# Optimization experiments

Hardware: AMD Instinct MI355X
Metric: run time of the kernel (lower is better)

Reference implementation:

```python
import jax, jax.numpy as jnp
import numpy as np

N_INST = 1_000_000
N_BINS_X = 512
N_BINS_Y = 512
STDDEV_X = 0.6
STDDEV_Y = 0.6
STDDEV_TRUNC = 2.5
NUM_CKSR = 48
NUM_CE = 96
SLICE_CAP = 16
SQRT2 = float(np.sqrt(2.0))
# truncated window spans 2*trunc*stddev = 3.0 bin units -> at most 5 bins per axis
K = 5


def setup_inputs() -> dict:
    key = jax.random.key(0)
    k1, k2, k3, k4, k5 = jax.random.split(key, 5)
    scale = jnp.array([N_BINS_X, N_BINS_Y], dtype=jnp.float32)
    inst_pos = jax.random.uniform(k1, (N_INST, 2), dtype=jnp.float32) * scale
    luts = jax.random.randint(k2, (N_INST,), 0, 7, dtype=jnp.int32)
    luts = jnp.where(luts == 1, 0, luts)  # assert: no LUT has type 1
    ffs = jax.random.randint(k3, (N_INST,), 0, 2, dtype=jnp.int32)
    ffs = jnp.where(luts > 0, 0, ffs)  # an instance is either a LUT or a FF
    cksr = jax.random.randint(k4, (N_INST,), 0, NUM_CKSR, dtype=jnp.int32)
    ce = jax.random.randint(k5, (N_INST,), 0, NUM_CE, dtype=jnp.int32)
    ff_ctrlsets = jnp.stack([cksr, ce], axis=1)
    return {"inst_pos": inst_pos, "is_inst_luts": luts, "is_inst_ffs": ffs,
            "ff_ctrlsets": ff_ctrlsets}


def _axis_weights(pos, stddev, num_bins):
    """Truncated-Gaussian bin overlap weights along one axis.
    pos: (N,) centers in bin units. Returns bins (N,K) int32, weights (N,K)."""
    half = STDDEV_TRUNC * stddev
    lo_bin = jnp.floor(pos - half).astype(jnp.int32)            # (N,)
    bins = lo_bin[:, None] + jnp.arange(K, dtype=jnp.int32)     # (N,K)
    e_lo = bins.astype(pos.dtype)
    e_hi = e_lo + 1.0
    w_lo = (pos - half)[:, None]
    w_hi = (pos + half)[:, None]
    lo_c = jnp.clip(e_lo, w_lo, w_hi)
    hi_c = jnp.clip(e_hi, w_lo, w_hi)
    phi = lambda e: 0.5 * (1.0 + jax.lax.erf((e - pos[:, None]) / (stddev * SQRT2)))
    w = phi(hi_c) - phi(lo_c)
    valid = (bins >= 0) & (bins < num_bins)
    w = jnp.where(valid, w, 0.0)
    w = w / (jnp.sum(w, axis=1, keepdims=True) + 1e-12)  # each inst contributes unit demand
    return jnp.clip(bins, 0, num_bins - 1), w


def reference(inst_pos, is_inst_luts, is_inst_ffs, ff_ctrlsets):
    dt = inst_pos.dtype
    bx, wx = _axis_weights(inst_pos[:, 0], STDDEV_X, N_BINS_X)
    by, wy = _axis_weights(inst_pos[:, 1], STDDEV_Y, N_BINS_Y)
    w2 = wx[:, :, None] * wy[:, None, :]                        # (N,K,K)
    idx = bx[:, :, None] * N_BINS_Y + by[:, None, :]            # (N,K,K) flat bin id
    nb = N_BINS_X * N_BINS_Y

    lut_mask = is_inst_luts > 0
    ff_mask = (is_inst_ffs > 0) & (~lut_mask)

    # LUT demand map (Gaussian splat of LUT instances)
    lut_w = jnp.where(lut_mask[:, None, None], w2, 0.0)
    lut_dem = jnp.zeros(nb, dt).at[idx.reshape(-1)].add(lut_w.reshape(-1))

    # FF demand maps keyed by control sets (cksr shared per half-slice, ce per quarter)
    ff_w = jnp.where(ff_mask[:, None, None], w2, 0.0)
    cksr = ff_ctrlsets[:, 0]
    ce = ff_ctrlsets[:, 1]
    idx_ck = (idx * NUM_CKSR + cksr[:, None, None]).reshape(-1)
    idx_ce = (idx * NUM_CE + ce[:, None, None]).reshape(-1)
    ck_dem = jnp.zeros(nb * NUM_CKSR, dt).at[idx_ck].add(ff_w.reshape(-1))
    ck_dem = ck_dem.reshape(nb, NUM_CKSR)
    ce_dem = jnp.zeros(nb * NUM_CE, dt).at[idx_ce].add(ff_w.reshape(-1))
    ce_dem = ce_dem.reshape(nb, NUM_CE)

    # ultrascale packing rule: half-slice shares CK/SR, quarter-slice shares CE
    half_cap = SLICE_CAP / 2.0
    quarter_cap = SLICE_CAP / 4.0
    eff_ck = jnp.sum(jnp.ceil(ck_dem / half_cap), axis=1) * half_cap
    eff_ce = jnp.sum(jnp.ceil(ce_dem / quarter_cap), axis=1) * quarter_cap
    ff_eff = jnp.maximum(eff_ck, eff_ce)        # effective FF capacity consumed per bin
    ff_raw = jnp.sum(ck_dem, axis=1)            # raw FF demand per bin
    ff_scale = jnp.maximum(ff_eff / jnp.maximum(ff_raw, 1e-6), 1.0)
    lut_scale = jnp.maximum(lut_dem / SLICE_CAP, 1.0)

    # gather per-instance inflated resource area with the same Gaussian weights
    lut_area = jnp.sum(w2 * lut_scale[idx], axis=(1, 2))
    ff_area = jnp.sum(w2 * ff_scale[idx], axis=(1, 2))
    zero = jnp.zeros((), dt)
    return jnp.where(lut_mask, lut_area, zero) + jnp.where(ff_mask, ff_area, zero)
```

## Files before the change

kernel.cpp:

```cpp
#include <hip/hip_runtime.h>

#define N_INST   1000000
#define NBX      512
#define NBY      512
#define NB       (NBX * NBY)
#define NUM_CKSR 48
#define NUM_CE   96
#define K        4

#define FTX   16
#define FTY   8
#define TGX   (NBX / FTX)
#define TGY   (NBY / FTY)
#define NFT   (TGX * TGY)
#define NBLK  512
#define NPER  (NFT / NBLK)
#define SUB   8
#define CAPL  96
#define CAPF  48
#define RS    145
#define ACCW  (FTX * FTY * RS)
#define PXW   20
#define PYW   12
#define PW    (PXW * PYW)

#define CSTRIDE 16

#define KHALF  ((float)(2.5 * 0.6))
#define KDENOM ((float)(0.6 * 1.4142135623730951))

__device__ __forceinline__ void axis_weights4(float pos, int nbins, int& lo_out, float w[K]) {
    float wlo = pos - KHALF;
    float whi = pos + KHALF;
    int lo_bin = (int)floorf(wlo);
    lo_out = lo_bin;
    float phi[K + 1];
#pragma unroll
    for (int k = 0; k <= K; ++k) {
        float e = (float)(lo_bin + k);
        float ec = fminf(fmaxf(e, wlo), whi);
        phi[k] = 0.5f * (1.f + erff((ec - pos) / KDENOM));
    }
    float wsum = 0.f;
#pragma unroll
    for (int k = 0; k < K; ++k) {
        int b = lo_bin + k;
        float ww = phi[k + 1] - phi[k];
        if (b < 0 || b >= nbins) ww = 0.f;
        w[k] = ww;
        wsum += ww;
    }
    float d = wsum + 1e-12f;
#pragma unroll
    for (int k = 0; k < K; ++k) w[k] = w[k] / d;
}

__device__ __forceinline__ unsigned q10(float w) {
    return min(1023u, (unsigned)rintf(w * 1024.f));
}

__global__ void __launch_bounds__(256) classify_kernel(
        const float* __restrict__ pos,
        const int* __restrict__ luts,
        const int* __restrict__ ffs,
        const int* __restrict__ ctrl,
        int* __restrict__ lut_cur,
        int* __restrict__ ff_cur,
        uint4* __restrict__ lutb,
        float4* __restrict__ ffwx,
        float4* __restrict__ ffwy,
        unsigned* __restrict__ ffmeta) {
    int i = blockIdx.x * blockDim.x + threadIdx.x;
    if (i >= N_INST) return;
    int sb = blockIdx.x & (SUB - 1);
    bool is_lut = luts[i] > 0;
    bool is_ff  = !is_lut && (ffs[i] > 0);
    if (!is_lut && !is_ff) return;

    float px = pos[2 * i], py = pos[2 * i + 1];
    int lox, loy;
    float wx[K], wy[K];
    axis_weights4(px, NBX, lox, wx);
    axis_weights4(py, NBY, loy, wy);

    if (is_lut) {
        unsigned qx[4] = { q10(wx[0]), q10(wx[1]), q10(wx[2]), q10(wx[3]) };
        unsigned qy[4] = { q10(wy[0]), q10(wy[1]), q10(wy[2]), q10(wy[3]) };
        int tx = ((int)px) >> 4, ty = ((int)py) >> 3;
        unsigned rx = (unsigned)(lox - tx * FTX + 2);
        unsigned ry = (unsigned)(loy - ty * FTY + 2);
        uint4 e;
        e.x = qx[0] | (qx[1] << 10) | (qx[2] << 20);
        e.y = qx[3] | (qy[0] << 10) | (qy[1] << 20);
        e.z = qy[2] | (qy[3] << 10);
        e.w = rx | (ry << 5);
        int sbk = (tx * TGY + ty) * SUB + sb;
        int slot = atomicAdd(&lut_cur[sbk * CSTRIDE], 1);
        if (slot < CAPL) lutb[(size_t)sbk * CAPL + slot] = e;
        return;
    }

    float4 w1 = make_float4(wx[0], wx[1], wx[2], wx[3]);
    float4 w2 = make_float4(wy[0], wy[1], wy[2], wy[3]);
    unsigned ck   = (unsigned)ctrl[2 * i];
    unsigned ce48 = 48u + (unsigned)ctrl[2 * i + 1];
    int tx0 = max(lox, 0) >> 4, tx1 = min(lox + 3, NBX - 1) >> 4;
    int ty0 = max(loy, 0) >> 3, ty1 = min(loy + 3, NBY - 1) >> 3;
    for (int tx = tx0; tx <= tx1; ++tx) {
        for (int ty = ty0; ty <= ty1; ++ty) {
            unsigned cx = (unsigned)(lox - tx * FTX + 4);
            unsigned cy = (unsigned)(loy - ty * FTY + 4);
            int sbk = (tx * TGY + ty) * SUB + sb;
            int slot = atomicAdd(&ff_cur[sbk * CSTRIDE], 1);
            if (slot < CAPF) {
                size_t idx = (size_t)sbk * CAPF + slot;
                ffwx[idx] = w1;
                ffwy[idx] = w2;
                ffmeta[idx] = ck | (ce48 << 6) | (cx << 14) | (cy << 19);
            }
        }
    }
}

__global__ void __launch_bounds__(1024) tile_kernel(
        const uint4* __restrict__ lutb,
        const float4* __restrict__ ffwx,
        const float4* __restrict__ ffwy,
        const unsigned* __restrict__ ffmeta,
        const int* __restrict__ lut_cur,
        const int* __restrict__ ff_cur,
        float* __restrict__ lut_dem,
        float* __restrict__ ff_scale) {
    __shared__ float acc[ACCW];
    __shared__ unsigned patch[PW];
    __shared__ int cnt_s[2 * SUB];
    __shared__ int lpre[SUB + 1], fpre[SUB + 1];
    int tid = threadIdx.x;

    for (int tt = 0; tt < NPER; ++tt) {
        int t = blockIdx.x + tt * NBLK;
        int X0 = (t / TGY) * FTX;
        int Y0 = (t % TGY) * FTY;

        if (tid < SUB)
            cnt_s[tid] = min(lut_cur[(t * SUB + tid) * CSTRIDE], CAPL);
        else if (tid < 2 * SUB)
            cnt_s[tid] = min(ff_cur[(t * SUB + (tid - SUB)) * CSTRIDE], CAPF);

        for (int j = tid; j < ACCW; j += 1024) acc[j] = 0.f;
        if (tid < PW) patch[tid] = 0u;
        __syncthreads();

        if (tid == 0) {
            int s = 0; lpre[0] = 0;
            for (int c = 0; c < SUB; ++c) { s += cnt_s[c]; lpre[c + 1] = s; }
        } else if (tid == 1) {
            int s = 0; fpre[0] = 0;
            for (int c = 0; c < SUB; ++c) { s += cnt_s[SUB + c]; fpre[c + 1] = s; }
        }
        __syncthreads();

        int ltot = lpre[SUB];
        for (int e = tid; e < ltot; e += 1024) {
            int c = 0;
#pragma unroll
            for (int k = 1; k < SUB; ++k) c += (e >= lpre[k]);
            uint4 a = lutb[((size_t)t * SUB + c) * CAPL + (e - lpre[c])];
            unsigned qx[4] = { a.x & 1023u, (a.x >> 10) & 1023u, (a.x >> 20) & 1023u, a.y & 1023u };
            unsigned qy[4] = { (a.y >> 10) & 1023u, (a.y >> 20) & 1023u, a.z & 1023u, (a.z >> 10) & 1023u };
            int base = (int)(a.w & 31u) * PYW + (int)((a.w >> 5) & 15u);
#pragma unroll
            for (int kx = 0; kx < K; ++kx) {
                int rb = base + kx * PYW;
#pragma unroll
                for (int ky = 0; ky < K; ++ky)
                    atomicAdd(&patch[rb + ky], qx[kx] * qy[ky]);
            }
        }

        int ftot = fpre[SUB];
        for (int e = tid; e < ftot; e += 1024) {
            int c = 0;
#pragma unroll
            for (int k = 1; k < SUB; ++k) c += (e >= fpre[k]);
            size_t idx = ((size_t)t * SUB + c) * CAPF + (e - fpre[c]);
            float4 a = ffwx[idx];
            float4 b = ffwy[idx];
            unsigned m = ffmeta[idx];
            float fx[4] = { a.x, a.y, a.z, a.w };
            float fy[4] = { b.x, b.y, b.z, b.w };
            int ck   = (int)(m & 63u);
            int ce48 = (int)((m >> 6) & 255u);
            int cx   = (int)((m >> 14) & 31u) - 4;
            int cy   = (int)((m >> 19) & 15u) - 4;
#pragma unroll
            for (int kx = 0; kx < K; ++kx) {
                int gx = cx + kx;
                if ((unsigned)gx >= FTX) continue;
                float wv = fx[kx];
#pragma unroll
                for (int ky = 0; ky < K; ++ky) {
                    int gy = cy + ky;
                    if ((unsigned)gy >= FTY) continue;
                    float w2 = wv * fy[ky];
                    if (w2 != 0.f) {
                        float* row = acc + (gx * FTY + gy) * RS;
                        unsafeAtomicAdd(row + ck, w2);
                        unsafeAtomicAdd(row + ce48, w2);
                    }
                }
            }
        }
        __syncthreads();

        if (tid < 512) {
            int lb = tid >> 2, q = tid & 3;
            const float* row = acc + lb * RS;
            float raw = 0.f, effck = 0.f, effce = 0.f;
#pragma unroll
            for (int c = 0; c < 12; ++c) {
                float v = row[12 * q + c];
                raw += v;
                effck += ceilf(v * 0.125f);
            }
#pragma unroll
            for (int c = 0; c < 24; ++c) {
                effce += ceilf(row[48 + 24 * q + c] * 0.25f);
            }
            raw   += __shfl_xor(raw, 1);   raw   += __shfl_xor(raw, 2);
            effck += __shfl_xor(effck, 1); effck += __shfl_xor(effck, 2);
            effce += __shfl_xor(effce, 1); effce += __shfl_xor(effce, 2);
            if (q == 0) {
                float eff = fmaxf(effck * 8.f, effce * 4.f);
                int gx = X0 + (lb >> 3);
                int gy = Y0 + (lb & 7);
                ff_scale[gx * NBY + gy] = fmaxf(eff / fmaxf(raw, 1e-6f), 1.f);
            }
        } else if (tid < 512 + PW) {
            int j = tid - 512;
            unsigned v = patch[j];
            if (v != 0u) {
                int gx = X0 - 2 + j / PYW;
                int gy = Y0 - 2 + j % PYW;
                if (gx >= 0 && gx < NBX && gy >= 0 && gy < NBY)
                    unsafeAtomicAdd(&lut_dem[gx * NBY + gy], (float)v * (1.f / 1048576.f));
            }
        }
        __syncthreads();
    }
}

__global__ void __launch_bounds__(256) area_kernel(
        const float* __restrict__ pos,
        const int* __restrict__ luts,
        const int* __restrict__ ffs,
        const float* __restrict__ lut_dem,
        const float* __restrict__ ff_scale,
        float* __restrict__ out) {
    int i = blockIdx.x * blockDim.x + threadIdx.x;
    if (i >= N_INST) return;
    bool is_lut = luts[i] > 0;
    bool is_ff  = (ffs[i] > 0) && !is_lut;
    if (!is_lut && !is_ff) { out[i] = 0.f; return; }

    float px = pos[2 * i], py = pos[2 * i + 1];
    int lox, loy;
    float wx[K], wy[K];
    axis_weights4(px, NBX, lox, wx);
    axis_weights4(py, NBY, loy, wy);

    const float* tbl = is_lut ? lut_dem : ff_scale;
    float acc = 0.f;
#pragma unroll
    for (int kx = 0; kx < K; ++kx) {
        int gx = min(max(lox + kx, 0), NBX - 1);
#pragma unroll
        for (int ky = 0; ky < K; ++ky) {
            int gy = min(max(loy + ky, 0), NBY - 1);
            float w2 = wx[kx] * wy[ky];
            float v = tbl[gx * NBY + gy];
            float sc = is_lut ? fmaxf(v * 0.0625f, 1.f) : v;
            acc += w2 * sc;
        }
    }
    out[i] = acc;
}

extern "C" void kernel_launch(void* const* d_in, const int* in_sizes, int n_in,
                              void* d_out, int out_size, void* d_ws, size_t ws_size,
                              hipStream_t stream) {
    const float* pos  = (const float*)d_in[0];
    const int*   luts = (const int*)d_in[1];
    const int*   ffs  = (const int*)d_in[2];
    const int*   ctrl = (const int*)d_in[3];
    float* out = (float*)d_out;

    int*      lut_cur  = (int*)d_ws;
    int*      ff_cur   = lut_cur + NFT * SUB * CSTRIDE;
    float*    lut_dem  = (float*)(ff_cur + NFT * SUB * CSTRIDE);
    float*    ff_scale = lut_dem + NB;
    uint4*    lutb     = (uint4*)(ff_scale + NB);
    float4*   ffwx     = (float4*)(lutb + (size_t)NFT * SUB * CAPL);
    float4*   ffwy     = ffwx + (size_t)NFT * SUB * CAPF;
    unsigned* ffmeta   = (unsigned*)(ffwy + (size_t)NFT * SUB * CAPF);

    hipMemsetAsync(d_ws, 0, (size_t)(2 * NFT * SUB * CSTRIDE + NB) * sizeof(int), stream);

    dim3 blk(256);
    dim3 grdI((N_INST + 255) / 256);

    classify_kernel<<<grdI, blk, 0, stream>>>(pos, luts, ffs, ctrl,
                                              lut_cur, ff_cur, lutb, ffwx, ffwy, ffmeta);
    tile_kernel<<<NBLK, dim3(1024), 0, stream>>>(lutb, ffwx, ffwy, ffmeta,
                                                 lut_cur, ff_cur, lut_dem, ff_scale);
    area_kernel<<<grdI, blk, 0, stream>>>(pos, luts, ffs, lut_dem, ff_scale, out);
}
```

Before: 126.6 us.

## Prefetch next tile's instance records into registers with fixed slot mapping

Replaces the shared-memory prefix-sum compaction of per-subtile counts with a fixed thread-to-slot mapping (each thread owns one capacity slot and checks it against the count). It also double-buffers the LUT/FF records and counts for the next tile in registers, so their global loads overlap with the current tile's shared-memory atomics. This removes one barrier and the serial prefix loop per tile. In exchange it uses more registers, and threads whose slots are empty sit idle instead of being compacted.

```diff
diff --git a/kernel.cpp b/kernel.cpp
--- a/kernel.cpp
+++ b/kernel.cpp
@@ -133,39 +133,65 @@
         float* __restrict__ ff_scale) {
     __shared__ float acc[ACCW];
     __shared__ unsigned patch[PW];
-    __shared__ int cnt_s[2 * SUB];
-    __shared__ int lpre[SUB + 1], fpre[SUB + 1];
     int tid = threadIdx.x;
 
+    const int  lsub  = tid / CAPL, lslot = tid - lsub * CAPL;
+    const int  fsub  = tid / CAPF, fslot = tid - fsub * CAPF;
+    const bool llane = tid < SUB * CAPL;
+    const bool flane = tid < SUB * CAPF;
+
+    int      lcnt[2] = {0, 0}, fcnt[2] = {0, 0};
+    uint4    le[2];
+    float4   fxr[2], fyr[2];
+    unsigned fmr[2];
+    le[0] = le[1] = make_uint4(0u, 0u, 0u, 0u);
+    fxr[0] = fxr[1] = make_float4(0.f, 0.f, 0.f, 0.f);
+    fyr[0] = fyr[1] = make_float4(0.f, 0.f, 0.f, 0.f);
+    fmr[0] = fmr[1] = 0u;
+
+    {
+        int t = blockIdx.x;
+        if (llane) {
+            lcnt[0] = lut_cur[(t * SUB + lsub) * CSTRIDE];
+            le[0]   = lutb[((size_t)t * SUB + lsub) * CAPL + lslot];
+        }
+        if (flane) {
+            fcnt[0] = ff_cur[(t * SUB + fsub) * CSTRIDE];
+            size_t fi = ((size_t)t * SUB + fsub) * CAPF + fslot;
+            fxr[0] = ffwx[fi];
+            fyr[0] = ffwy[fi];
+            fmr[0] = ffmeta[fi];
+        }
+    }
+
+#pragma unroll
     for (int tt = 0; tt < NPER; ++tt) {
+        const int cur = tt & 1, nxt = cur ^ 1;
         int t = blockIdx.x + tt * NBLK;
         int X0 = (t / TGY) * FTX;
         int Y0 = (t % TGY) * FTY;
 
-        if (tid < SUB)
-            cnt_s[tid] = min(lut_cur[(t * SUB + tid) * CSTRIDE], CAPL);
-        else if (tid < 2 * SUB)
-            cnt_s[tid] = min(ff_cur[(t * SUB + (tid - SUB)) * CSTRIDE], CAPF);
-
         for (int j = tid; j < ACCW; j += 1024) acc[j] = 0.f;
         if (tid < PW) patch[tid] = 0u;
+
+        if (tt + 1 < NPER) {
+            int tn = blockIdx.x + (tt + 1) * NBLK;
+            if (llane) {
+                lcnt[nxt] = lut_cur[(tn * SUB + lsub) * CSTRIDE];
+                le[nxt]   = lutb[((size_t)tn * SUB + lsub) * CAPL + lslot];
+            }
+            if (flane) {
+                fcnt[nxt] = ff_cur[(tn * SUB + fsub) * CSTRIDE];
+                size_t fi = ((size_t)tn * SUB + fsub) * CAPF + fslot;
+                fxr[nxt] = ffwx[fi];
+                fyr[nxt] = ffwy[fi];
+                fmr[nxt] = ffmeta[fi];
+            }
+        }
         __syncthreads();
 
-        if (tid == 0) {
-            int s = 0; lpre[0] = 0;
-            for (int c = 0; c < SUB; ++c) { s += cnt_s[c]; lpre[c + 1] = s; }
-        } else if (tid == 1) {
-            int s = 0; fpre[0] = 0;
-            for (int c = 0; c < SUB; ++c) { s += cnt_s[SUB + c]; fpre[c + 1] = s; }
-        }
-        __syncthreads();
-
-        int ltot = lpre[SUB];
-        for (int e = tid; e < ltot; e += 1024) {
-            int c = 0;
-#pragma unroll
-            for (int k = 1; k < SUB; ++k) c += (e >= lpre[k]);
-            uint4 a = lutb[((size_t)t * SUB + c) * CAPL + (e - lpre[c])];
+        if (llane && lslot < min(lcnt[cur], CAPL)) {
+            uint4 a = le[cur];
             unsigned qx[4] = { a.x & 1023u, (a.x >> 10) & 1023u, (a.x >> 20) & 1023u, a.y & 1023u };
             unsigned qy[4] = { (a.y >> 10) & 1023u, (a.y >> 20) & 1023u, a.z & 1023u, (a.z >> 10) & 1023u };
             int base = (int)(a.w & 31u) * PYW + (int)((a.w >> 5) & 15u);
@@ -178,15 +204,10 @@
             }
         }
 
-        int ftot = fpre[SUB];
-        for (int e = tid; e < ftot; e += 1024) {
-            int c = 0;
-#pragma unroll
-            for (int k = 1; k < SUB; ++k) c += (e >= fpre[k]);
-            size_t idx = ((size_t)t * SUB + c) * CAPF + (e - fpre[c]);
-            float4 a = ffwx[idx];
-            float4 b = ffwy[idx];
-            unsigned m = ffmeta[idx];
+        if (flane && fslot < min(fcnt[cur], CAPF)) {
+            float4 a = fxr[cur];
+            float4 b = fyr[cur];
+            unsigned m = fmr[cur];
             float fx[4] = { a.x, a.y, a.z, a.w };
             float fy[4] = { b.x, b.y, b.z, b.w };
             int ck   = (int)(m & 63u);
```

New measurement: 129.6 us. +2.4%, slower.
